# Optimization experiments

Hardware: AMD Instinct MI355X
Metric: run time of the kernel (lower is better)

The kernel has to match this reference:

```python
import jax, jax.numpy as jnp
import numpy as np

HIDDEN = 2048
N_HEADS = 16
N_KV_HEADS = 8
HEAD_DIM = 128
MROPE_SECTION = [8, 8, 24, 24]          # sums to HEAD_DIM // 2
ROPE_THETA = 10000.0
B, S, CTX = 4, 1024, 2048
# per-frequency section index (which of the 4 position streams drives each freq)
_SEC_IDX = np.repeat(np.arange(len(MROPE_SECTION)), MROPE_SECTION)  # (HEAD_DIM//2,)


def setup_inputs() -> dict:
    key = jax.random.key(0)
    ks = jax.random.split(key, 6)
    return {
        "hidden_states": jax.random.normal(ks[0], (B, S, HIDDEN), jnp.float32),
        "Wqkv": jax.random.normal(ks[1], (HIDDEN, (N_HEADS + 2 * N_KV_HEADS) * HEAD_DIM), jnp.float32) * 0.02,
        "Wo": jax.random.normal(ks[2], (N_HEADS * HEAD_DIM, HIDDEN), jnp.float32) * 0.02,
        "ctx_k": jax.random.normal(ks[3], (B, CTX, N_KV_HEADS, HEAD_DIM), jnp.float32),
        "ctx_v": jax.random.normal(ks[4], (B, CTX, N_KV_HEADS, HEAD_DIM), jnp.float32),
        "position_ids": jax.random.randint(ks[5], (len(MROPE_SECTION), S), 0, CTX + S, jnp.int32),
    }


def _mrope_cos_sin(position_ids):
    # position_ids: (n_sections, S) int -> cos/sin of shape (S, HEAD_DIM)
    half = HEAD_DIM // 2
    inv_freq = 1.0 / (ROPE_THETA ** (jnp.arange(0, half, dtype=jnp.float32) * 2.0 / HEAD_DIM))
    freqs = position_ids.astype(jnp.float32)[:, :, None] * inv_freq[None, None, :]  # (4, S, half)
    sec = jnp.asarray(_SEC_IDX)[None, None, :]                                       # (1, 1, half)
    f = jnp.take_along_axis(freqs, jnp.broadcast_to(sec, (1,) + freqs.shape[1:]), axis=0)[0]  # (S, half)
    emb = jnp.concatenate([f, f], axis=-1)  # (S, HEAD_DIM)
    return jnp.cos(emb), jnp.sin(emb)


def _rotate_half(x):
    h = x.shape[-1] // 2
    return jnp.concatenate([-x[..., h:], x[..., :h]], axis=-1)


def reference(hidden_states, Wqkv, Wo, ctx_k, ctx_v, position_ids):
    b, s, _ = hidden_states.shape
    q_size = N_HEADS * HEAD_DIM
    kv_size = N_KV_HEADS * HEAD_DIM
    qkv = hidden_states @ Wqkv  # (B, S, q+2kv)
    q = qkv[..., :q_size].reshape(b, s, N_HEADS, HEAD_DIM)
    k = qkv[..., q_size:q_size + kv_size].reshape(b, s, N_KV_HEADS, HEAD_DIM)
    v = qkv[..., q_size + kv_size:].reshape(b, s, N_KV_HEADS, HEAD_DIM)

    cos, sin = _mrope_cos_sin(position_ids)        # (S, D) each
    cos = cos[None, :, None, :]
    sin = sin[None, :, None, :]
    q = q * cos + _rotate_half(q) * sin
    k = k * cos + _rotate_half(k) * sin

    # KV-cache concat along sequence dim
    k = jnp.concatenate([ctx_k, k], axis=1)        # (B, CTX+S, KV, D)
    v = jnp.concatenate([ctx_v, v], axis=1)

    # GQA: expand kv heads to query heads
    rep = N_HEADS // N_KV_HEADS
    k = jnp.repeat(k, rep, axis=2)                 # (B, T, H, D)
    v = jnp.repeat(v, rep, axis=2)

    scale = HEAD_DIM ** -0.5
    scores = jnp.einsum("bqhd,bkhd->bhqk", q, k) * scale  # non-causal
    probs = jax.nn.softmax(scores, axis=-1)
    out = jnp.einsum("bhqk,bkhd->bqhd", probs, v)  # (B, S, H, D)
    out = out.reshape(b, s, N_HEADS * HEAD_DIM)
    return out @ Wo
```

## Files before the change

kernel.cpp:

```cpp
#include <hip/hip_runtime.h>
#include <hip/hip_bf16.h>
#include <stdint.h>

#define NH 16
#define NKV 8
#define HD 128
#define BB 4
#define SS 1024
#define CTXL 2048
#define LT 3072
#define HID 2048
#define QKVN 4096
#define MROWS 4096

typedef __hip_bfloat16 bf16;
using f32x4 = __attribute__((ext_vector_type(4))) float;
using s16x8 = __attribute__((ext_vector_type(8))) short;

#define MFMA(a, b, c) __builtin_amdgcn_mfma_f32_16x16x32_bf16((a), (b), (c), 0, 0, 0)

__device__ __forceinline__ void gload_lds16(const void* g, void* l) {
  __builtin_amdgcn_global_load_lds((const __attribute__((address_space(1))) void*)g,
                                   (__attribute__((address_space(3))) void*)l, 16, 0, 0);
}

__device__ __forceinline__ void store_bf8(bf16* dst, const float* f) {
  bf16 tmp[8];
#pragma unroll
  for (int j = 0; j < 8; ++j) tmp[j] = __float2bfloat16(f[j]);
  __builtin_memcpy((void*)dst, (const void*)tmp, 16);
}

__device__ __forceinline__ float bf2f(short x) {
  unsigned int u = ((unsigned int)(unsigned short)x) << 16;
  float f;
  __builtin_memcpy(&f, &u, 4);
  return f;
}

#define P1_CVT 4096
#define P1_WQ (P1_CVT + 8192)
#define P1_WO (P1_WQ + 4096)
#define P1_RT (P1_WO + 256)
#define P1_CK (P1_RT + 4096)
#define P1_CV (P1_CK + 8192)

__global__ void prep1(const float* __restrict__ hs, const float* __restrict__ Wqkv,
                      const float* __restrict__ Wo, const float* __restrict__ ck,
                      const float* __restrict__ cv, const int* __restrict__ pid,
                      bf16* __restrict__ Hb, bf16* __restrict__ WqT,
                      bf16* __restrict__ WoT, bf16* __restrict__ Kf,
                      bf16* __restrict__ Vt, float* __restrict__ cosT,
                      float* __restrict__ sinT) {
  __shared__ float tile[32][33];
  const int blk = blockIdx.x, thr = threadIdx.x;
  if (blk < P1_CVT) {
    size_t tid = (size_t)blk * 256 + thr;
    const float4* p = (const float4*)(hs + tid * 8);
    float4 a = p[0], b = p[1];
    float f[8] = {a.x, a.y, a.z, a.w, b.x, b.y, b.z, b.w};
    store_bf8(Hb + tid * 8, f);
  } else if (blk < P1_WQ) {
    int j = blk - P1_CVT;
    int c0 = (j & 127) * 32, r0 = (j >> 7) * 32;
    int tx = thr & 31, ty = thr >> 5;
#pragma unroll
    for (int i = 0; i < 32; i += 8)
      tile[ty + i][tx] = Wqkv[(size_t)(r0 + ty + i) * QKVN + c0 + tx];
    __syncthreads();
#pragma unroll
    for (int i = 0; i < 32; i += 8)
      WqT[(size_t)(c0 + ty + i) * HID + r0 + tx] = __float2bfloat16(tile[tx][ty + i]);
  } else if (blk < P1_WO) {
    int j = blk - P1_WQ;
    int c0 = (j & 63) * 32, r0 = (j >> 6) * 32;
    int tx = thr & 31, ty = thr >> 5;
#pragma unroll
    for (int i = 0; i < 32; i += 8)
      tile[ty + i][tx] = Wo[(size_t)(r0 + ty + i) * 2048 + c0 + tx];
    __syncthreads();
#pragma unroll
    for (int i = 0; i < 32; i += 8)
      WoT[(size_t)(c0 + ty + i) * 2048 + r0 + tx] = __float2bfloat16(tile[tx][ty + i]);
  } else if (blk < P1_RT) {
    int tid = (blk - P1_WO) * 256 + thr;
    int j = tid & 63, s = tid >> 6;
    int sec = (j < 8) ? 0 : (j < 16) ? 1 : (j < 40) ? 2 : 3;
    float pos = (float)pid[sec * SS + s];
    float inv = __expf(-(float)j * 0.14391156831212787f);
    float a = pos * inv;
    cosT[tid] = cosf(a);
    sinT[tid] = sinf(a);
  } else if (blk < P1_CK) {
    int tid = (blk - P1_RT) * 256 + thr;
    int d8 = tid & 15, l = (tid >> 4) & 2047, h = (tid >> 15) & 7, b = tid >> 18;
    const float* s = ck + (((size_t)b * CTXL + l) * NKV + h) * HD + d8 * 8;
    const float4* p = (const float4*)s;
    float4 a = p[0], bb = p[1];
    float f[8] = {a.x, a.y, a.z, a.w, bb.x, bb.y, bb.z, bb.w};
    store_bf8(Kf + (((size_t)(b * NKV + h)) * LT + l) * HD + d8 * 8, f);
  } else {
    int j = blk - P1_CK;
    int l0 = (j & 63) * 32, d0 = ((j >> 6) & 3) * 32;
    int bz = j >> 8, b = bz >> 3, h = bz & 7;
    int tx = thr & 31, ty = thr >> 5;
#pragma unroll
    for (int i = 0; i < 32; i += 8)
      tile[ty + i][tx] =
          cv[(((size_t)b * CTXL + l0 + ty + i) * NKV + h) * HD + d0 + tx];
    __syncthreads();
#pragma unroll
    for (int i = 0; i < 32; i += 8)
      Vt[(((size_t)(b * NKV + h)) * HD + d0 + ty + i) * LT + l0 + tx] =
          __float2bfloat16(tile[tx][ty + i]);
  }
}

__global__ void prep2(const bf16* __restrict__ qkv, const float* __restrict__ cosT,
                      const float* __restrict__ sinT, bf16* __restrict__ Kf,
                      bf16* __restrict__ Vt) {
  __shared__ float tile[32][33];
  const int blk = blockIdx.x, thr = threadIdx.x;
  if (blk < 8192) {
    int tid = blk * 256 + thr;
    int j = tid & 63, h = (tid >> 6) & 7, s = (tid >> 9) & 1023, b = tid >> 19;
    const bf16* src = qkv + ((size_t)b * SS + s) * QKVN + 2048 + h * HD;
    float x1 = __bfloat162float(src[j]), x2 = __bfloat162float(src[j + 64]);
    float c = cosT[s * 64 + j], sn = sinT[s * 64 + j];
    bf16* dst = Kf + (((size_t)(b * NKV + h)) * LT + CTXL + s) * HD;
    dst[j] = __float2bfloat16(x1 * c - x2 * sn);
    dst[j + 64] = __float2bfloat16(x2 * c + x1 * sn);
  } else {
    int j = blk - 8192;
    int s0 = (j & 31) * 32, d0 = ((j >> 5) & 3) * 32;
    int bz = j >> 7, b = bz >> 3, h = bz & 7;
    int tx = thr & 31, ty = thr >> 5;
#pragma unroll
    for (int i = 0; i < 32; i += 8)
      tile[ty + i][tx] = __bfloat162float(
          qkv[((size_t)b * SS + s0 + ty + i) * QKVN + 3072 + h * HD + d0 + tx]);
    __syncthreads();
#pragma unroll
    for (int i = 0; i < 32; i += 8)
      Vt[(((size_t)(b * NKV + h)) * HD + d0 + ty + i) * LT + CTXL + s0 + tx] =
          __float2bfloat16(tile[tx][ty + i]);
  }
}

template <typename OT>
__global__ __launch_bounds__(512, 1) void gemm_bt(const bf16* __restrict__ A,
                                                  const bf16* __restrict__ BT,
                                                  OT* __restrict__ C, int M, int N,
                                                  int K) {
  __shared__ __attribute__((aligned(16))) bf16 lA[3][256][64];
  __shared__ __attribute__((aligned(16))) bf16 lB[3][128][64];
  const int t = threadIdx.x;
  const int lane = t & 63, w = t >> 6;
  const int wr = w >> 1, wc = w & 1;
  const int lrow = lane & 15, kgrp = lane >> 4;
  const int rchk = lrow & 7;
  const int lin = blockIdx.y * gridDim.x + blockIdx.x;
  const int qq = (gridDim.x * gridDim.y) >> 3;
  const int swz = (lin & 7) * qq + (lin >> 3);
  const int bx = swz % gridDim.x, by = swz / gridDim.x;
  const int m0 = by * 256, n0 = bx * 128;
  const int srow = lane >> 3;
  const int schk = (lane & 7) ^ srow;
  const f32x4 fz = {0.f, 0.f, 0.f, 0.f};
  f32x4 acc[4][4];
#pragma unroll
  for (int i = 0; i < 4; ++i)
#pragma unroll
    for (int j = 0; j < 4; ++j) acc[i][j] = fz;
  const int NTK = K >> 6;

#define GSTAGE(ib, kt)                                                      \
  do {                                                                      \
    _Pragma("unroll") for (int c = 0; c < 4; ++c) {                         \
      int ra = c * 64 + w * 8 + srow;                                       \
      gload_lds16(A + (size_t)(m0 + ra) * K + (kt)*64 + schk * 8,           \
                  &lA[ib][c * 64 + w * 8][0]);                              \
    }                                                                       \
    _Pragma("unroll") for (int c = 0; c < 2; ++c) {                         \
      int rb = c * 64 + w * 8 + srow;                                       \
      gload_lds16(BT + (size_t)(n0 + rb) * K + (kt)*64 + schk * 8,          \
                  &lB[ib][c * 64 + w * 8][0]);                              \
    }                                                                       \
  } while (0)

  GSTAGE(0, 0);
  GSTAGE(1, 1);
  int ib = 0;
  for (int kt = 0; kt < NTK; ++kt) {
    if (kt + 1 < NTK)
      asm volatile("s_waitcnt vmcnt(6) lgkmcnt(0)" ::: "memory");
    else
      asm volatile("s_waitcnt vmcnt(0) lgkmcnt(0)" ::: "memory");
    __builtin_amdgcn_s_barrier();
    __builtin_amdgcn_sched_barrier(0);
    if (kt + 2 < NTK) {
      int ib2 = ib + 2;
      if (ib2 >= 3) ib2 -= 3;
      GSTAGE(ib2, kt + 2);
    }
#pragma unroll
    for (int kk = 0; kk < 2; ++kk) {
      s16x8 af[4], bf[4];
#pragma unroll
      for (int i = 0; i < 4; ++i)
        af[i] = *(const s16x8*)&lA[ib][wr * 64 + i * 16 + lrow]
                                     [(((kk << 2) + kgrp) ^ rchk) * 8];
#pragma unroll
      for (int j = 0; j < 4; ++j)
        bf[j] = *(const s16x8*)&lB[ib][wc * 64 + j * 16 + lrow]
                                     [(((kk << 2) + kgrp) ^ rchk) * 8];
      __builtin_amdgcn_s_setprio(1);
#pragma unroll
      for (int i = 0; i < 4; ++i)
#pragma unroll
        for (int j = 0; j < 4; ++j) acc[i][j] = MFMA(af[i], bf[j], acc[i][j]);
      __builtin_amdgcn_s_setprio(0);
    }
    ++ib;
    if (ib >= 3) ib = 0;
  }
#undef GSTAGE

#pragma unroll
  for (int i = 0; i < 4; ++i)
#pragma unroll
    for (int j = 0; j < 4; ++j)
#pragma unroll
      for (int r = 0; r < 4; ++r) {
        int row = m0 + wr * 64 + i * 16 + kgrp * 4 + r;
        int col = n0 + wc * 64 + j * 16 + lrow;
        float v = acc[i][j][r];
        if constexpr (sizeof(OT) == 2)
          C[(size_t)row * N + col] = __float2bfloat16(v);
        else
          C[(size_t)row * N + col] = v;
      }
}


#define PSTR 72
#define KVB 128
#define NTT 24
#define SCALE2 0.1275174335919605f

__global__ __launch_bounds__(512, 2) void flash_attn(
    const bf16* __restrict__ qkv, const float* __restrict__ cosT,
    const float* __restrict__ sinT, const bf16* __restrict__ Kf,
    const bf16* __restrict__ Vt, bf16* __restrict__ O) {
  __shared__ __attribute__((aligned(16))) bf16 Kl[2][128][128];
  __shared__ __attribute__((aligned(16))) bf16 Vl[2][128][128];
  __shared__ __attribute__((aligned(16))) bf16 P_lds[8][16][PSTR];
  const int t = threadIdx.x, lane = t & 63, w = t >> 6;
  const int id = blockIdx.x;
  const int b = id >> 6, hk = id & 7;
  const int h = (hk << 1) | ((id >> 5) & 1);
  const int qb = (id >> 3) & 3;
  const int lrow = lane & 15, kgrp = lane >> 4;
  const bf16* Kp = Kf + (size_t)(b * NKV + hk) * LT * HD;
  const bf16* Vp = Vt + (size_t)(b * NKV + hk) * HD * LT;

  s16x8 qf[2][4];
#pragma unroll
  for (int f = 0; f < 2; ++f) {
    int srw_i = qb * 256 + w * 32 + f * 16 + lrow;
    const bf16* qrow = qkv + ((size_t)b * SS + srw_i) * QKVN + h * HD;
    s16x8 qr[4];
#pragma unroll
    for (int kd = 0; kd < 4; ++kd)
      qr[kd] = *(const s16x8*)&qrow[kd * 32 + kgrp * 8];
    const float* crow = cosT + srw_i * 64 + kgrp * 8;
    const float* srow = sinT + srw_i * 64 + kgrp * 8;
    float qv[4][8], cc[2][8], ssv[2][8];
#pragma unroll
    for (int kd = 0; kd < 4; ++kd)
#pragma unroll
      for (int j = 0; j < 8; ++j) qv[kd][j] = bf2f(qr[kd][j]);
#pragma unroll
    for (int g = 0; g < 2; ++g)
#pragma unroll
      for (int j = 0; j < 8; ++j) {
        cc[g][j] = crow[g * 32 + j];
        ssv[g][j] = srow[g * 32 + j];
      }
    bf16 o[4][8];
#pragma unroll
    for (int j = 0; j < 8; ++j) {
      o[0][j] = __float2bfloat16(qv[0][j] * cc[0][j] - qv[2][j] * ssv[0][j]);
      o[1][j] = __float2bfloat16(qv[1][j] * cc[1][j] - qv[3][j] * ssv[1][j]);
      o[2][j] = __float2bfloat16(qv[2][j] * cc[0][j] + qv[0][j] * ssv[0][j]);
      o[3][j] = __float2bfloat16(qv[3][j] * cc[1][j] + qv[1][j] * ssv[1][j]);
    }
#pragma unroll
    for (int kd = 0; kd < 4; ++kd) __builtin_memcpy(&qf[f][kd], o[kd], 16);
  }

  const f32x4 fz = {0.f, 0.f, 0.f, 0.f};
  f32x4 acc[2][8];
#pragma unroll
  for (int f = 0; f < 2; ++f)
#pragma unroll
    for (int i = 0; i < 8; ++i) acc[f][i] = fz;
  float m_[2] = {-1e30f, -1e30f}, l_[2] = {0.f, 0.f};

#define STAGE_K(buf, l0)                                                        \
  do {                                                                          \
    _Pragma("unroll") for (int c = 0; c < 4; ++c) {                             \
      int row = w * 16 + c * 4 + (lane >> 4);                                   \
      gload_lds16(Kp + (size_t)((l0) + row) * HD + ((lane & 15) ^ (row & 15)) * 8, \
                  &Kl[buf][w * 16 + c * 4][0]);                                 \
    }                                                                           \
  } while (0)
#define STAGE_V(buf, l0)                                                        \
  do {                                                                          \
    _Pragma("unroll") for (int c = 0; c < 4; ++c) {                             \
      int d = w * 16 + c * 4 + (lane >> 4);                                     \
      gload_lds16(Vp + (size_t)d * LT + (l0) + ((lane & 15) ^ (d & 15)) * 8,    \
                  &Vl[buf][w * 16 + c * 4][0]);                                 \
    }                                                                           \
  } while (0)

  STAGE_K(0, 0);
  STAGE_V(0, 0);
  __syncthreads();

  for (int tt = 0; tt < NTT; ++tt) {
    const int cur = tt & 1;
    if (tt + 1 < NTT) {
      STAGE_K(cur ^ 1, (tt + 1) * KVB);
      STAGE_V(cur ^ 1, (tt + 1) * KVB);
    }

    f32x4 sc[2][8];
#pragma unroll
    for (int f = 0; f < 2; ++f)
#pragma unroll
      for (int cf = 0; cf < 8; ++cf) sc[f][cf] = fz;
#pragma unroll
    for (int cf = 0; cf < 8; ++cf)
#pragma unroll
      for (int kd = 0; kd < 4; ++kd) {
        s16x8 kb =
            *(const s16x8*)&Kl[cur][cf * 16 + lrow][((kd * 4 + kgrp) ^ lrow) * 8];
#pragma unroll
        for (int f = 0; f < 2; ++f) sc[f][cf] = MFMA(kb, qf[f][kd], sc[f][cf]);
      }

    float mxv[2];
#pragma unroll
    for (int f = 0; f < 2; ++f) {
      float mx = sc[f][0][0];
#pragma unroll
      for (int cf = 0; cf < 8; ++cf)
#pragma unroll
        for (int r = 0; r < 4; ++r) mx = fmaxf(mx, sc[f][cf][r]);
      mx *= SCALE2;
      mx = fmaxf(mx, __shfl_xor(mx, 16, 64));
      mx = fmaxf(mx, __shfl_xor(mx, 32, 64));
      mxv[f] = mx;
    }
    bool nb = (mxv[0] > m_[0] + 8.f) || (mxv[1] > m_[1] + 8.f);
    if (__any(nb)) {
#pragma unroll
      for (int f = 0; f < 2; ++f) {
        float mn = fmaxf(m_[f], mxv[f]);
        float so = exp2f(m_[f] - mn);
        m_[f] = mn;
        l_[f] *= so;
        float sob[4];
#pragma unroll
        for (int r = 0; r < 4; ++r) sob[r] = __shfl(so, kgrp * 4 + r, 16);
#pragma unroll
        for (int nd = 0; nd < 8; ++nd)
#pragma unroll
          for (int r = 0; r < 4; ++r) acc[f][nd][r] *= sob[r];
      }
    }

    float lp[2] = {0.f, 0.f};
#pragma unroll
    for (int half = 0; half < 2; ++half) {
      s16x8 pa[2][2];
#pragma unroll
      for (int f = 0; f < 2; ++f) {
#pragma unroll
        for (int cf = 0; cf < 4; ++cf) {
          int cfs = half * 4 + cf;
          bf16 pk[4];
#pragma unroll
          for (int r = 0; r < 4; ++r) {
            float p = exp2f(sc[f][cfs][r] * SCALE2 - m_[f]);
            lp[f] += p;
            pk[r] = __float2bfloat16(p);
          }
          __builtin_memcpy((void*)&P_lds[w][lrow][cf * 16 + kgrp * 4], pk, 8);
        }
#pragma unroll
        for (int kc = 0; kc < 2; ++kc)
          pa[f][kc] = *(const s16x8*)&P_lds[w][lrow][kc * 32 + kgrp * 8];
      }
#pragma unroll
      for (int nd = 0; nd < 8; ++nd)
#pragma unroll
        for (int kc = 0; kc < 2; ++kc) {
          s16x8 vb = *(const s16x8*)&Vl[cur][nd * 16 + lrow]
                                       [((half * 8 + kc * 4 + kgrp) ^ lrow) * 8];
#pragma unroll
          for (int f = 0; f < 2; ++f) acc[f][nd] = MFMA(pa[f][kc], vb, acc[f][nd]);
        }
    }
#pragma unroll
    for (int f = 0; f < 2; ++f) l_[f] += lp[f];

    __syncthreads();
  }
#undef STAGE_K
#undef STAGE_V

  float li[2][4];
#pragma unroll
  for (int f = 0; f < 2; ++f) {
    float lv = l_[f];
    lv += __shfl_xor(lv, 16, 64);
    lv += __shfl_xor(lv, 32, 64);
#pragma unroll
    for (int r = 0; r < 4; ++r) li[f][r] = 1.f / __shfl(lv, kgrp * 4 + r, 16);
  }
#pragma unroll
  for (int f = 0; f < 2; ++f)
#pragma unroll
    for (int nd = 0; nd < 8; ++nd)
#pragma unroll
      for (int r = 0; r < 4; ++r) {
        int row = qb * 256 + w * 32 + f * 16 + kgrp * 4 + r;
        O[((size_t)b * SS + row) * 2048 + h * HD + nd * 16 + lrow] =
            __float2bfloat16(acc[f][nd][r] * li[f][r]);
      }
}


extern "C" void kernel_launch(void* const* d_in, const int* in_sizes, int n_in,
                              void* d_out, int out_size, void* d_ws, size_t ws_size,
                              hipStream_t stream) {
  const float* hs = (const float*)d_in[0];
  const float* Wqkv = (const float*)d_in[1];
  const float* Wo = (const float*)d_in[2];
  const float* ctx_k = (const float*)d_in[3];
  const float* ctx_v = (const float*)d_in[4];
  const int* pid = (const int*)d_in[5];
  float* out = (float*)d_out;
  char* ws = (char*)d_ws;

  bf16* Hb = (bf16*)(ws);
  bf16* WqT = (bf16*)(ws + 16777216);
  bf16* WoT = (bf16*)(ws + 33554432);
  bf16* qkv = (bf16*)(ws + 41943040);
  bf16* Kfull = (bf16*)(ws + 92274688);
  bf16* Vt = (bf16*)(ws + 117440512);
  float* cosT = (float*)(ws + 142606336);
  float* sinT = (float*)(ws + 142606336 + 262144);
  bf16* attn = Hb;

  prep1<<<P1_CV, 256, 0, stream>>>(hs, Wqkv, Wo, ctx_k, ctx_v, pid, Hb, WqT, WoT,
                                   Kfull, Vt, cosT, sinT);
  gemm_bt<bf16><<<dim3(QKVN / 128, MROWS / 256), 512, 0, stream>>>(
      Hb, WqT, qkv, MROWS, QKVN, HID);
  prep2<<<12288, 256, 0, stream>>>(qkv, cosT, sinT, Kfull, Vt);
  flash_attn<<<256, 512, 0, stream>>>(qkv, cosT, sinT, Kfull, Vt, attn);
  gemm_bt<float><<<dim3(2048 / 128, MROWS / 256), 512, 0, stream>>>(
      attn, WoT, out, MROWS, 2048, HID);
}
```

Baseline: 317.7 us.

## Fuse K RoPE and V transpose into QKV GEMM epilogue, drop prep2

Adds a dedicated QKV GEMM whose epilogue stages the accumulator tile in LDS. For K-head column tiles it applies mRoPE and writes directly into the K cache buffer, and for V tiles it writes transposed into Vt. Q tiles are still written to qkv as before. This removes the separate prep2 launch and its round trip of K/V through global memory, at the cost of a larger LDS footprint and extra epilogue syncs and serial work in the GEMM.

```diff
diff --git a/kernel.cpp b/kernel.cpp
--- a/kernel.cpp
+++ b/kernel.cpp
@@ -116,34 +116,136 @@
   }
 }
 
-__global__ void prep2(const bf16* __restrict__ qkv, const float* __restrict__ cosT,
-                      const float* __restrict__ sinT, bf16* __restrict__ Kf,
-                      bf16* __restrict__ Vt) {
-  __shared__ float tile[32][33];
-  const int blk = blockIdx.x, thr = threadIdx.x;
-  if (blk < 8192) {
-    int tid = blk * 256 + thr;
-    int j = tid & 63, h = (tid >> 6) & 7, s = (tid >> 9) & 1023, b = tid >> 19;
-    const bf16* src = qkv + ((size_t)b * SS + s) * QKVN + 2048 + h * HD;
-    float x1 = __bfloat162float(src[j]), x2 = __bfloat162float(src[j + 64]);
-    float c = cosT[s * 64 + j], sn = sinT[s * 64 + j];
-    bf16* dst = Kf + (((size_t)(b * NKV + h)) * LT + CTXL + s) * HD;
-    dst[j] = __float2bfloat16(x1 * c - x2 * sn);
-    dst[j + 64] = __float2bfloat16(x2 * c + x1 * sn);
+
+__global__ __launch_bounds__(512, 1) void gemm_qkv(
+    const bf16* __restrict__ A, const bf16* __restrict__ BT,
+    bf16* __restrict__ qkv, bf16* __restrict__ Kf, bf16* __restrict__ Vt,
+    const float* __restrict__ cosT, const float* __restrict__ sinT) {
+  __shared__ __attribute__((aligned(16))) char smem[147456];
+  bf16* lA = (bf16*)smem;
+  bf16* lB = (bf16*)(smem + 98304);
+  const int K = HID, N = QKVN;
+  const int t = threadIdx.x;
+  const int lane = t & 63, w = t >> 6;
+  const int wr = w >> 1, wc = w & 1;
+  const int lrow = lane & 15, kgrp = lane >> 4;
+  const int rchk = lrow & 7;
+  const int lin = blockIdx.y * gridDim.x + blockIdx.x;
+  const int qq = (gridDim.x * gridDim.y) >> 3;
+  const int swz = (lin & 7) * qq + (lin >> 3);
+  const int bx = swz % gridDim.x, by = swz / gridDim.x;
+  const int m0 = by * 256, n0 = bx * 128;
+  const int srow = lane >> 3;
+  const int schk = (lane & 7) ^ srow;
+  const f32x4 fz = {0.f, 0.f, 0.f, 0.f};
+  f32x4 acc[4][4];
+#pragma unroll
+  for (int i = 0; i < 4; ++i)
+#pragma unroll
+    for (int j = 0; j < 4; ++j) acc[i][j] = fz;
+  const int NTK = K >> 6;
+
+#define GSTAGE(ib, kt)                                                      \
+  do {                                                                      \
+    _Pragma("unroll") for (int c = 0; c < 4; ++c) {                         \
+      int ra = c * 64 + w * 8 + srow;                                       \
+      gload_lds16(A + (size_t)(m0 + ra) * K + (kt)*64 + schk * 8,           \
+                  &lA[((ib)*256 + c * 64 + w * 8) * 64]);                   \
+    }                                                                       \
+    _Pragma("unroll") for (int c = 0; c < 2; ++c) {                         \
+      int rb = c * 64 + w * 8 + srow;                                       \
+      gload_lds16(BT + (size_t)(n0 + rb) * K + (kt)*64 + schk * 8,          \
+                  &lB[((ib)*128 + c * 64 + w * 8) * 64]);                   \
+    }                                                                       \
+  } while (0)
+
+  GSTAGE(0, 0);
+  GSTAGE(1, 1);
+  int ib = 0;
+  for (int kt = 0; kt < NTK; ++kt) {
+    if (kt + 1 < NTK)
+      asm volatile("s_waitcnt vmcnt(6) lgkmcnt(0)" ::: "memory");
+    else
+      asm volatile("s_waitcnt vmcnt(0) lgkmcnt(0)" ::: "memory");
+    __builtin_amdgcn_s_barrier();
+    __builtin_amdgcn_sched_barrier(0);
+    if (kt + 2 < NTK) {
+      int ib2 = ib + 2;
+      if (ib2 >= 3) ib2 -= 3;
+      GSTAGE(ib2, kt + 2);
+    }
+#pragma unroll
+    for (int kk = 0; kk < 2; ++kk) {
+      s16x8 af[4], bf[4];
+#pragma unroll
+      for (int i = 0; i < 4; ++i)
+        af[i] = *(const s16x8*)&lA[((ib)*256 + wr * 64 + i * 16 + lrow) * 64 +
+                                   (((kk << 2) + kgrp) ^ rchk) * 8];
+#pragma unroll
+      for (int j = 0; j < 4; ++j)
+        bf[j] = *(const s16x8*)&lB[((ib)*128 + wc * 64 + j * 16 + lrow) * 64 +
+                                   (((kk << 2) + kgrp) ^ rchk) * 8];
+      __builtin_amdgcn_s_setprio(1);
+#pragma unroll
+      for (int i = 0; i < 4; ++i)
+#pragma unroll
+        for (int j = 0; j < 4; ++j) acc[i][j] = MFMA(af[i], bf[j], acc[i][j]);
+      __builtin_amdgcn_s_setprio(0);
+    }
+    ++ib;
+    if (ib >= 3) ib = 0;
+  }
+#undef GSTAGE
+
+  const int nt = n0 >> 7;
+  const int b = m0 >> 10, s0 = m0 & 1023;
+  if (nt < 16) {
+#pragma unroll
+    for (int i = 0; i < 4; ++i)
+#pragma unroll
+      for (int j = 0; j < 4; ++j)
+#pragma unroll
+        for (int r = 0; r < 4; ++r) {
+          int row = m0 + wr * 64 + i * 16 + kgrp * 4 + r;
+          int col = n0 + wc * 64 + j * 16 + lrow;
+          qkv[(size_t)row * N + col] = __float2bfloat16(acc[i][j][r]);
+        }
   } else {
-    int j = blk - 8192;
-    int s0 = (j & 31) * 32, d0 = ((j >> 5) & 3) * 32;
-    int bz = j >> 7, b = bz >> 3, h = bz & 7;
-    int tx = thr & 31, ty = thr >> 5;
-#pragma unroll
-    for (int i = 0; i < 32; i += 8)
-      tile[ty + i][tx] = __bfloat162float(
-          qkv[((size_t)b * SS + s0 + ty + i) * QKVN + 3072 + h * HD + d0 + tx]);
     __syncthreads();
-#pragma unroll
-    for (int i = 0; i < 32; i += 8)
-      Vt[(((size_t)(b * NKV + h)) * HD + d0 + ty + i) * LT + CTXL + s0 + tx] =
-          __float2bfloat16(tile[tx][ty + i]);
+    float* stage = (float*)smem;
+#pragma unroll
+    for (int i = 0; i < 4; ++i)
+#pragma unroll
+      for (int j = 0; j < 4; ++j)
+#pragma unroll
+        for (int r = 0; r < 4; ++r)
+          stage[(wr * 64 + i * 16 + kgrp * 4 + r) * 129 + wc * 64 + j * 16 + lrow] =
+              acc[i][j][r];
+    __syncthreads();
+    if (nt < 24) {
+      const int h = nt - 16;
+#pragma unroll 4
+      for (int it = 0; it < 32; ++it) {
+        int idx = it * 512 + t;
+        int r = idx >> 6, j = idx & 63;
+        float x1 = stage[r * 129 + j], x2 = stage[r * 129 + j + 64];
+        int s = s0 + r;
+        float c = cosT[s * 64 + j], sn = sinT[s * 64 + j];
+        bf16* dst = Kf + ((size_t)(b * NKV + h) * LT + CTXL + s) * HD;
+        dst[j] = __float2bfloat16(x1 * c - x2 * sn);
+        dst[j + 64] = __float2bfloat16(x2 * c + x1 * sn);
+      }
+    } else {
+      const int h = nt - 24;
+#pragma unroll 4
+      for (int it = 0; it < 64; ++it) {
+        int idx = it * 512 + t;
+        int soff = idx & 255, d = idx >> 8;
+        float v = stage[soff * 129 + d];
+        Vt[((size_t)(b * NKV + h) * HD + d) * LT + CTXL + s0 + soff] =
+            __float2bfloat16(v);
+      }
+    }
   }
 }
 
@@ -242,7 +344,6 @@
       }
 }
 
-
 #define PSTR 72
 #define KVB 128
 #define NTT 24
@@ -467,9 +568,8 @@
 
   prep1<<<P1_CV, 256, 0, stream>>>(hs, Wqkv, Wo, ctx_k, ctx_v, pid, Hb, WqT, WoT,
                                    Kfull, Vt, cosT, sinT);
-  gemm_bt<bf16><<<dim3(QKVN / 128, MROWS / 256), 512, 0, stream>>>(
-      Hb, WqT, qkv, MROWS, QKVN, HID);
-  prep2<<<12288, 256, 0, stream>>>(qkv, cosT, sinT, Kfull, Vt);
+  gemm_qkv<<<dim3(QKVN / 128, MROWS / 256), 512, 0, stream>>>(
+      Hb, WqT, qkv, Kfull, Vt, cosT, sinT);
   flash_attn<<<256, 512, 0, stream>>>(qkv, cosT, sinT, Kfull, Vt, attn);
   gemm_bt<float><<<dim3(2048 / 128, MROWS / 256), 512, 0, stream>>>(
       attn, WoT, out, MROWS, 2048, HID);
```

Result: faster. 302.0 us (-4.9%).

## Fuse K RoPE and V transpose into a new 256x256 QKV GEMM epilogue

Applied to the files above, without the earlier changes.

Replaces the generic QKV GEMM plus the separate prep2 kernel with a dedicated gemm_qkv kernel. It uses 256x256 tiles, double-buffered LDS with split half-tile staging and phased MFMA, and applies RoPE to K and transposes V directly from accumulators staged through LDS. This removes a full write and re-read of the K/V part of qkv and one kernel launch. The trade-off is a larger LDS footprint (~129KB), halving the grid to 256 blocks, which may underfill the GPU's CUs, and extra epilogue synchronisation.

```diff
diff --git a/kernel.cpp b/kernel.cpp
--- a/kernel.cpp
+++ b/kernel.cpp
@@ -116,35 +116,159 @@
   }
 }
 
-__global__ void prep2(const bf16* __restrict__ qkv, const float* __restrict__ cosT,
-                      const float* __restrict__ sinT, bf16* __restrict__ Kf,
-                      bf16* __restrict__ Vt) {
-  __shared__ float tile[32][33];
-  const int blk = blockIdx.x, thr = threadIdx.x;
-  if (blk < 8192) {
-    int tid = blk * 256 + thr;
-    int j = tid & 63, h = (tid >> 6) & 7, s = (tid >> 9) & 1023, b = tid >> 19;
-    const bf16* src = qkv + ((size_t)b * SS + s) * QKVN + 2048 + h * HD;
-    float x1 = __bfloat162float(src[j]), x2 = __bfloat162float(src[j + 64]);
-    float c = cosT[s * 64 + j], sn = sinT[s * 64 + j];
-    bf16* dst = Kf + (((size_t)(b * NKV + h)) * LT + CTXL + s) * HD;
-    dst[j] = __float2bfloat16(x1 * c - x2 * sn);
-    dst[j + 64] = __float2bfloat16(x2 * c + x1 * sn);
+
+__global__ __launch_bounds__(512, 1) void gemm_qkv(
+    const bf16* __restrict__ A, const bf16* __restrict__ BT,
+    bf16* __restrict__ qkv, bf16* __restrict__ Kf, bf16* __restrict__ Vt,
+    const float* __restrict__ cosT, const float* __restrict__ sinT) {
+  __shared__ __attribute__((aligned(16))) char smem[132096];
+  bf16* lds = (bf16*)smem;
+#define lAp(s, hf) (lds + ((s)*2 + (hf)) * 8192)
+#define lBp(s, hf) (lds + 32768 + ((s)*2 + (hf)) * 8192)
+  const int K = HID;
+  const int t = threadIdx.x;
+  const int lane = t & 63, w = t >> 6;
+  const int wr = w >> 2, wc = w & 3;
+  const int lrow = lane & 15, kgrp = lane >> 4;
+  const int lin = blockIdx.y * gridDim.x + blockIdx.x;
+  const int qq = (gridDim.x * gridDim.y) >> 3;
+  const int swz = (lin & 7) * qq + (lin >> 3);
+  const int bx = swz % gridDim.x, by = swz / gridDim.x;
+  const int m0 = by * 256, n0 = bx * 256;
+  const f32x4 fz = {0.f, 0.f, 0.f, 0.f};
+  f32x4 acc[8][4];
+#pragma unroll
+  for (int i = 0; i < 8; ++i)
+#pragma unroll
+    for (int j = 0; j < 4; ++j) acc[i][j] = fz;
+
+#define STAGEH(sslot, skt, isB, shalf)                                        \
+  do {                                                                        \
+    _Pragma("unroll") for (int c = 0; c < 2; ++c) {                           \
+      int row = w * 16 + c * 8 + (lane >> 3);                                 \
+      int sch = (lane & 7) ^ (lane >> 3);                                     \
+      const bf16* src =                                                       \
+          (isB) ? (BT + (size_t)(n0 + (shalf)*128 + row) * K + (skt)*64 + sch * 8) \
+                : (A + (size_t)(m0 + (shalf)*128 + row) * K + (skt)*64 + sch * 8); \
+      bf16* dst = ((isB) ? lBp((sslot), (shalf)) : lAp((sslot), (shalf))) +   \
+                  (w * 16 + c * 8) * 64;                                      \
+      gload_lds16(src, dst);                                                  \
+    }                                                                         \
+  } while (0)
+
+#define PHASE(cslot, qm, qn, DOST, sslot, skt, isB, shalf)                    \
+  do {                                                                        \
+    if (DOST) {                                                               \
+      STAGEH(sslot, skt, isB, shalf);                                         \
+      asm volatile("s_waitcnt vmcnt(2)" ::: "memory");                        \
+    } else {                                                                  \
+      asm volatile("s_waitcnt vmcnt(0)" ::: "memory");                        \
+    }                                                                         \
+    __builtin_amdgcn_s_barrier();                                             \
+    __builtin_amdgcn_sched_barrier(0);                                        \
+    s16x8 af_[4][2], bf_[2][2];                                               \
+    _Pragma("unroll") for (int fi = 0; fi < 4; ++fi)                          \
+        _Pragma("unroll") for (int ks = 0; ks < 2; ++ks) {                    \
+      int row = (qm)*64 + fi * 16 + lrow;                                     \
+      af_[fi][ks] = *(const s16x8*)&lAp(cslot, wr)[row * 64 +                 \
+                                                   ((ks * 4 + kgrp) ^ (lrow & 7)) * 8]; \
+    }                                                                         \
+    _Pragma("unroll") for (int fj = 0; fj < 2; ++fj)                          \
+        _Pragma("unroll") for (int ks = 0; ks < 2; ++ks) {                    \
+      int col = (wc & 1) * 64 + (qn)*32 + fj * 16 + lrow;                     \
+      bf_[fj][ks] = *(const s16x8*)&lBp(cslot, wc >> 1)[col * 64 +            \
+                                                        ((ks * 4 + kgrp) ^ (lrow & 7)) * 8]; \
+    }                                                                         \
+    asm volatile("s_waitcnt lgkmcnt(0)" ::: "memory");                        \
+    __builtin_amdgcn_sched_barrier(0);                                        \
+    __builtin_amdgcn_s_setprio(1);                                            \
+    _Pragma("unroll") for (int fi = 0; fi < 4; ++fi)                          \
+        _Pragma("unroll") for (int fj = 0; fj < 2; ++fj)                      \
+            _Pragma("unroll") for (int ks = 0; ks < 2; ++ks)                  \
+                acc[(qm)*4 + fi][(qn)*2 + fj] =                               \
+        MFMA(af_[fi][ks], bf_[fj][ks], acc[(qm)*4 + fi][(qn)*2 + fj]);        \
+    __builtin_amdgcn_s_setprio(0);                                            \
+    __builtin_amdgcn_s_barrier();                                             \
+  } while (0)
+
+  STAGEH(0, 0, 0, 0);
+  STAGEH(0, 0, 1, 0);
+  STAGEH(0, 0, 0, 1);
+  STAGEH(0, 0, 1, 1);
+  asm volatile("s_waitcnt vmcnt(0)" ::: "memory");
+  __builtin_amdgcn_s_barrier();
+
+  for (int kt = 0; kt < 32; kt += 2) {
+    PHASE(0, 0, 0, true, 1, kt + 1, 0, 0);
+    PHASE(0, 1, 0, true, 1, kt + 1, 1, 0);
+    PHASE(0, 0, 1, true, 1, kt + 1, 0, 1);
+    PHASE(0, 1, 1, true, 1, kt + 1, 1, 1);
+    const bool d2 = (kt + 2 < 32);
+    PHASE(1, 0, 0, d2, 0, kt + 2, 0, 0);
+    PHASE(1, 1, 0, d2, 0, kt + 2, 1, 0);
+    PHASE(1, 0, 1, d2, 0, kt + 2, 0, 1);
+    PHASE(1, 1, 1, d2, 0, kt + 2, 1, 1);
+  }
+#undef PHASE
+#undef STAGEH
+
+  const int b = m0 >> 10, s0 = m0 & 1023;
+  if (n0 < 2048) {
+#pragma unroll
+    for (int fm = 0; fm < 8; ++fm)
+#pragma unroll
+      for (int fn = 0; fn < 4; ++fn)
+#pragma unroll
+        for (int r = 0; r < 4; ++r) {
+          int row = m0 + wr * 128 + fm * 16 + kgrp * 4 + r;
+          int col = n0 + wc * 64 + fn * 16 + lrow;
+          qkv[(size_t)row * QKVN + col] = __float2bfloat16(acc[fm][fn][r]);
+        }
   } else {
-    int j = blk - 8192;
-    int s0 = (j & 31) * 32, d0 = ((j >> 5) & 3) * 32;
-    int bz = j >> 7, b = bz >> 3, h = bz & 7;
-    int tx = thr & 31, ty = thr >> 5;
-#pragma unroll
-    for (int i = 0; i < 32; i += 8)
-      tile[ty + i][tx] = __bfloat162float(
-          qkv[((size_t)b * SS + s0 + ty + i) * QKVN + 3072 + h * HD + d0 + tx]);
-    __syncthreads();
-#pragma unroll
-    for (int i = 0; i < 32; i += 8)
-      Vt[(((size_t)(b * NKV + h)) * HD + d0 + ty + i) * LT + CTXL + s0 + tx] =
-          __float2bfloat16(tile[tx][ty + i]);
-  }
+    float* stage = (float*)smem;
+#pragma unroll 1
+    for (int hh = 0; hh < 2; ++hh) {
+      __syncthreads();
+      if ((wc >> 1) == hh) {
+#pragma unroll
+        for (int fm = 0; fm < 8; ++fm)
+#pragma unroll
+          for (int fn = 0; fn < 4; ++fn)
+#pragma unroll
+            for (int r = 0; r < 4; ++r) {
+              int rr = wr * 128 + fm * 16 + kgrp * 4 + r;
+              int cc = (wc & 1) * 64 + fn * 16 + lrow;
+              stage[rr * 129 + cc] = acc[fm][fn][r];
+            }
+      }
+      __syncthreads();
+      if (n0 < 3072) {
+        int h = ((n0 - 2048) >> 7) + hh;
+#pragma unroll 4
+        for (int it = 0; it < 32; ++it) {
+          int idx = it * 512 + t;
+          int r = idx >> 6, j = idx & 63;
+          float x1 = stage[r * 129 + j], x2 = stage[r * 129 + j + 64];
+          int s = s0 + r;
+          float c = cosT[s * 64 + j], sn = sinT[s * 64 + j];
+          bf16* dst = Kf + ((size_t)(b * NKV + h) * LT + CTXL + s) * HD;
+          dst[j] = __float2bfloat16(x1 * c - x2 * sn);
+          dst[j + 64] = __float2bfloat16(x2 * c + x1 * sn);
+        }
+      } else {
+        int h = ((n0 - 3072) >> 7) + hh;
+#pragma unroll 4
+        for (int it = 0; it < 64; ++it) {
+          int idx = it * 512 + t;
+          int soff = idx & 255, d = idx >> 8;
+          Vt[((size_t)(b * NKV + h) * HD + d) * LT + CTXL + s0 + soff] =
+              __float2bfloat16(stage[soff * 129 + d]);
+        }
+      }
+    }
+  }
+#undef lAp
+#undef lBp
 }
 
 template <typename OT>
@@ -242,7 +366,6 @@
       }
 }
 
-
 #define PSTR 72
 #define KVB 128
 #define NTT 24
@@ -467,9 +590,8 @@
 
   prep1<<<P1_CV, 256, 0, stream>>>(hs, Wqkv, Wo, ctx_k, ctx_v, pid, Hb, WqT, WoT,
                                    Kfull, Vt, cosT, sinT);
-  gemm_bt<bf16><<<dim3(QKVN / 128, MROWS / 256), 512, 0, stream>>>(
-      Hb, WqT, qkv, MROWS, QKVN, HID);
-  prep2<<<12288, 256, 0, stream>>>(qkv, cosT, sinT, Kfull, Vt);
+  gemm_qkv<<<dim3(QKVN / 256, MROWS / 256), 512, 0, stream>>>(
+      Hb, WqT, qkv, Kfull, Vt, cosT, sinT);
   flash_attn<<<256, 512, 0, stream>>>(qkv, cosT, sinT, Kfull, Vt, attn);
   gemm_bt<float><<<dim3(2048 / 128, MROWS / 256), 512, 0, stream>>>(
       attn, WoT, out, MROWS, 2048, HID);
```

Result: faster. 292.6 us (-7.9%).
